# Kernel optimization log

Hardware: AMD Instinct MI355X
Metric: run time of the kernel (lower is better)

The kernel has to match this reference:

```python
import jax, jax.numpy as jnp
import numpy as np

B, T, D_IN, D_OUT, D_Z, D_H = 1024, 512, 64, 32, 32, 128
MIN_LV, MAX_LV = -10.0, 2.0
LOG2PI = float(np.log(2.0 * np.pi))
BETA_KL = 1.0


def _clamp(lv):
    return jnp.clip(lv, MIN_LV, MAX_LV)


def _mlp3(h, W1, b1, W2, b2, W3, b3):
    # depth=2 MLP: Linear->Tanh->Linear->Tanh->Linear
    h = jnp.tanh(h @ W1 + b1)
    h = jnp.tanh(h @ W2 + b2)
    return h @ W3 + b3


def setup_inputs() -> dict:
    key = jax.random.key(0)
    ks = iter(jax.random.split(key, 40))

    def lin(i, o):
        W = jax.random.normal(next(ks), (i, o), jnp.float32) / np.sqrt(i)
        b = 0.01 * jax.random.normal(next(ks), (o,), jnp.float32)
        return W, b

    inp = {}
    inp["x"] = jax.random.normal(next(ks), (B, T, D_IN), jnp.float32)
    inp["y_true"] = jax.random.normal(next(ks), (B, T, D_OUT), jnp.float32)
    for name, i, o in [("prior", D_Z + D_IN, 2 * D_Z),
                       ("post", D_Z + D_IN + D_OUT, 2 * D_Z),
                       ("emit", D_Z, 2 * D_OUT)]:
        W1, b1 = lin(i, D_H)
        W2, b2 = lin(D_H, D_H)
        W3, b3 = lin(D_H, o)
        inp[f"{name}_W1"], inp[f"{name}_b1"] = W1, b1
        inp[f"{name}_W2"], inp[f"{name}_b2"] = W2, b2
        inp[f"{name}_W3"], inp[f"{name}_b3"] = W3, b3
    inp["z0_mu"] = jnp.zeros((D_Z,), jnp.float32)
    inp["z0_logvar"] = jnp.zeros((D_Z,), jnp.float32)
    return inp


def reference(x, y_true,
              prior_W1, prior_b1, prior_W2, prior_b2, prior_W3, prior_b3,
              post_W1, post_b1, post_W2, post_b2, post_W3, post_b3,
              emit_W1, emit_b1, emit_W2, emit_b2, emit_W3, emit_b3,
              z0_mu, z0_logvar):
    Bc, Tc = x.shape[0], x.shape[1]
    # deterministic reparameterization noise (torch uses randn_like)
    ek = jax.random.key(42)
    eps0 = jax.random.normal(jax.random.fold_in(ek, 0), (Bc, D_Z), jnp.float32)
    eps = jax.random.normal(jax.random.fold_in(ek, 1), (Tc, Bc, D_Z), jnp.float32)

    z0 = z0_mu + jnp.exp(0.5 * _clamp(z0_logvar)) * eps0  # (B, Z)
    xs = jnp.swapaxes(x, 0, 1)       # (T, B, D_in)
    ys = jnp.swapaxes(y_true, 0, 1)  # (T, B, D_out)

    def step(z_prev, inp_t):
        x_t, y_t, e_t = inp_t
        p = _mlp3(jnp.concatenate([z_prev, x_t], -1),
                  prior_W1, prior_b1, prior_W2, prior_b2, prior_W3, prior_b3)
        mu_p, lv_p = jnp.split(p, 2, -1)
        lv_p = _clamp(lv_p)
        q = _mlp3(jnp.concatenate([z_prev, x_t, y_t], -1),
                  post_W1, post_b1, post_W2, post_b2, post_W3, post_b3)
        mu_q, lv_q = jnp.split(q, 2, -1)
        lv_q = _clamp(lv_q)
        z_t = mu_q + jnp.exp(0.5 * lv_q) * e_t
        em = _mlp3(z_t, emit_W1, emit_b1, emit_W2, emit_b2, emit_W3, emit_b3)
        mu_y, lv_y = jnp.split(em, 2, -1)
        lv_y = _clamp(lv_y)
        return z_t, (mu_y, lv_y, mu_q, lv_q, mu_p, lv_p)

    _, (mu_y, lv_y, mu_q, lv_q, mu_p, lv_p) = jax.lax.scan(step, z0, (xs, ys, eps))
    mu_y = jnp.swapaxes(mu_y, 0, 1)  # (B, T, D_out) == y_hat (sample=False)
    lv_y = jnp.swapaxes(lv_y, 0, 1)

    # Gaussian NLL (mean over B*T, sum over out_dim)
    nll = 0.5 * jnp.mean(jnp.sum(lv_y + (y_true - mu_y) ** 2 / jnp.exp(lv_y) + LOG2PI, -1))
    # KL(q || p) diag Gaussians (mean over T*B, sum over latent)
    var_q, var_p = jnp.exp(lv_q), jnp.exp(lv_p)
    kl = 0.5 * jnp.mean(jnp.sum(lv_p - lv_q + (var_q + (mu_q - mu_p) ** 2) / (var_p + 1e-12) - 1.0, -1))
    total = nll + BETA_KL * kl
    return mu_y, total, nll, kl
```

## Files before the change

kernel.cpp:

```cpp
#include <hip/hip_runtime.h>
#include <stdint.h>

#define Bdim 1024
#define Tdim 512
#define DIN  64
#define DOUT 32
#define DZ   32
#define DH   128
#define Msamp 4
#define NWG  256
#define NTHR 512
#define SP   144

using s16x8 = __attribute__((ext_vector_type(8))) short;
using f32x4 = __attribute__((ext_vector_type(4))) float;

#define MFMA(a, b, c) __builtin_amdgcn_mfma_f32_16x16x32_bf16((a), (b), (c), 0, 0, 0)

#define BAR() do { asm volatile("s_waitcnt lgkmcnt(0)" ::: "memory"); \
                   __builtin_amdgcn_s_barrier();                      \
                   asm volatile("" ::: "memory"); } while (0)

__host__ __device__ inline void tf2x32(unsigned k0, unsigned k1, unsigned c0, unsigned c1,
                                       unsigned &o0, unsigned &o1) {
  unsigned ks2 = k0 ^ k1 ^ 0x1BD11BDAu;
  unsigned x0 = c0 + k0, x1 = c1 + k1;
#define TFR(r) { x0 += x1; x1 = (x1 << (r)) | (x1 >> (32 - (r))); x1 ^= x0; }
  TFR(13) TFR(15) TFR(26) TFR(6)
  x0 += k1;  x1 += ks2 + 1u;
  TFR(17) TFR(29) TFR(16) TFR(24)
  x0 += ks2; x1 += k0 + 2u;
  TFR(13) TFR(15) TFR(26) TFR(6)
  x0 += k0;  x1 += k1 + 3u;
  TFR(17) TFR(29) TFR(16) TFR(24)
  x0 += k1;  x1 += ks2 + 4u;
  TFR(13) TFR(15) TFR(26) TFR(6)
  x0 += ks2; x1 += k0 + 5u;
#undef TFR
  o0 = x0; o1 = x1;
}

__device__ inline float erfinv_xla(float x) {
  float w = -log1pf(-x * x);
  float p;
  if (w < 5.0f) {
    w -= 2.5f;
    p = 2.81022636e-08f;
    p = fmaf(p, w, 3.43273939e-07f);
    p = fmaf(p, w, -3.5233877e-06f);
    p = fmaf(p, w, -4.39150654e-06f);
    p = fmaf(p, w, 0.00021858087f);
    p = fmaf(p, w, -0.00125372503f);
    p = fmaf(p, w, -0.00417768164f);
    p = fmaf(p, w, 0.246640727f);
    p = fmaf(p, w, 1.50140941f);
  } else {
    w = sqrtf(w) - 3.0f;
    p = -0.000200214257f;
    p = fmaf(p, w, 0.000100950558f);
    p = fmaf(p, w, 0.00134934322f);
    p = fmaf(p, w, -0.00367342844f);
    p = fmaf(p, w, 0.00573950773f);
    p = fmaf(p, w, -0.0076224613f);
    p = fmaf(p, w, 0.00943887047f);
    p = fmaf(p, w, 1.00167406f);
    p = fmaf(p, w, 2.83297682f);
  }
  return p * x;
}

__device__ inline float bits_to_normal(unsigned bits) {
  float f = __uint_as_float((bits >> 9) | 0x3f800000u) - 1.0f;
  float u = f * 2.0f - 0.99999994f;
  u = fmaxf(u, -0.99999994f);
  return 1.41421356f * erfinv_xla(u);
}

__device__ inline float jax_normal(unsigned k0, unsigned k1, unsigned idx) {
  unsigned o0, o1;
  tf2x32(k0, k1, 0u, idx, o0, o1);
  return bits_to_normal(o0 ^ o1);
}

__device__ inline float clampf(float v) { return fminf(fmaxf(v, -10.0f), 2.0f); }
__device__ inline float tanh_fast(float v) {
  float e = __expf(2.0f * v);
  return 1.0f - __fdividef(2.0f, e + 1.0f);
}
__device__ inline short f2bf(float x) {
  unsigned u = __float_as_uint(x);
  u = (u + 0x7fffu + ((u >> 16) & 1u)) >> 16;
  return (short)u;
}
__device__ inline float sel4(f32x4 v, int g) {
  float r = v[0];
  r = (g == 1) ? v[1] : r;
  r = (g == 2) ? v[2] : r;
  r = (g == 3) ? v[3] : r;
  return r;
}

__device__ inline s16x8 load_frag(const float* __restrict__ W, int N, int kt, int nt, int lane) {
  int k0 = kt * 32 + ((lane >> 4) << 3);
  int n  = nt * 16 + (lane & 15);
  s16x8 f;
#pragma unroll
  for (int e = 0; e < 8; ++e) f[e] = f2bf(W[(size_t)(k0 + e) * N + n]);
  return f;
}

__global__ __launch_bounds__(NTHR, 2) void dssm_main(
    const float* __restrict__ gx, const float* __restrict__ gy,
    const float* __restrict__ pW1, const float* __restrict__ pb1,
    const float* __restrict__ pW2, const float* __restrict__ pb2,
    const float* __restrict__ pW3, const float* __restrict__ pb3,
    const float* __restrict__ qW1, const float* __restrict__ qb1,
    const float* __restrict__ qW2, const float* __restrict__ qb2,
    const float* __restrict__ qW3, const float* __restrict__ qb3,
    const float* __restrict__ eW1, const float* __restrict__ eb1,
    const float* __restrict__ eW2, const float* __restrict__ eb2,
    const float* __restrict__ eW3, const float* __restrict__ eb3,
    const float* __restrict__ z0mu, const float* __restrict__ z0lv,
    float* __restrict__ gout, float* __restrict__ gws,
    unsigned ka0, unsigned ka1, unsigned kb0, unsigned kb1)
{
  __shared__ __align__(16) short in_pq[4 * SP];
  __shared__ __align__(16) short hpa[4 * SP], hqa[4 * SP], hea[4 * SP];
  __shared__ __align__(16) short hpb[4 * SP], hqb[4 * SP], heb[4 * SP];
  __shared__ float out_q2[4][32][2], out_p2[4][32][2], emit_o2[4][32][2];
  __shared__ float y_f32[4][128];
  __shared__ float epsb[2][128];

  const int tid  = threadIdx.x;
  const int w    = tid >> 6;
  const int lane = tid & 63;
  const int col  = lane & 15;
  const int g    = lane >> 4;
  const int wg   = blockIdx.x;
  const int base = wg * Msamp;

  s16x8 f1p[3], f1q[4], f1e, f2[16], f3[8];
#pragma unroll
  for (int i = 0; i < 16; ++i) f2[i] = (s16x8)(short)0;
#pragma unroll
  for (int i = 0; i < 8; ++i) f3[i] = (s16x8)(short)0;

#pragma unroll
  for (int kt = 0; kt < 3; ++kt) f1p[kt] = load_frag(pW1, DH, kt, w, lane);
#pragma unroll
  for (int kt = 0; kt < 4; ++kt) f1q[kt] = load_frag(qW1, DH, kt, w, lane);
  f1e = load_frag(eW1, DH, 0, w, lane);

  if (w < 2) {
#pragma unroll
    for (int nt = 0; nt < 4; ++nt)
#pragma unroll
      for (int kt = 0; kt < 4; ++kt) f2[nt * 4 + kt] = load_frag(pW2, DH, kt, w * 4 + nt, lane);
  } else if (w < 4) {
#pragma unroll
    for (int nt = 0; nt < 4; ++nt)
#pragma unroll
      for (int kt = 0; kt < 4; ++kt) f2[nt * 4 + kt] = load_frag(qW2, DH, kt, (w - 2) * 4 + nt, lane);
  } else if (w < 6) {
#pragma unroll
    for (int nt = 0; nt < 4; ++nt)
#pragma unroll
      for (int kt = 0; kt < 4; ++kt) f2[nt * 4 + kt] = load_frag(eW2, DH, kt, (w - 4) * 4 + nt, lane);
  }

  if (w < 4) {
#pragma unroll
    for (int kt = 0; kt < 4; ++kt) f3[kt] = load_frag(eW3, 2 * DOUT, kt, w, lane);
  } else if (w < 6) {
#pragma unroll
    for (int kt = 0; kt < 4; ++kt) { f3[kt] = load_frag(qW3, 2 * DZ, kt, w - 4, lane);
                                     f3[4 + kt] = load_frag(qW3, 2 * DZ, kt, w - 2, lane); }
  } else {
#pragma unroll
    for (int kt = 0; kt < 4; ++kt) { f3[kt] = load_frag(pW3, 2 * DZ, kt, w - 6, lane);
                                     f3[4 + kt] = load_frag(pW3, 2 * DZ, kt, w - 4, lane); }
  }

  const float b1p = pb1[w * 16 + col], b1q = qb1[w * 16 + col], b1e = eb1[w * 16 + col];
  float b2[4];
#pragma unroll
  for (int nt = 0; nt < 4; ++nt) {
    int n = ((w & 1) * 4 + nt) * 16 + col;
    b2[nt] = (w < 2) ? pb2[n] : (w < 4) ? qb2[n] : (w < 6) ? eb2[n] : 0.0f;
  }
  float b3a = 0.0f, b3b = 0.0f;
  if (w < 4)      { b3a = eb3[w * 16 + col]; }
  else if (w < 6) { b3a = qb3[(w - 4) * 16 + col]; b3b = qb3[32 + (w - 4) * 16 + col]; }
  else            { b3a = pb3[(w - 6) * 16 + col]; b3b = pb3[32 + (w - 6) * 16 + col]; }

  const s16x8* A1 = (const s16x8*)(in_pq + (col & 3) * SP) + g;
  const short* p2s = (w < 2) ? hpa : (w < 4) ? hqa : hea;
  const s16x8* A2 = (const s16x8*)(p2s + (col & 3) * SP) + g;
  short* p2d = (w < 2) ? hpb : (w < 4) ? hqb : heb;
  const short* p3s = (w < 4) ? heb : (w < 6) ? hqb : hpb;
  const s16x8* A3 = (const s16x8*)(p3s + (col & 3) * SP) + g;

  if (w < 4) {
    in_pq[w * SP + 32 + lane] = f2bf(gx[((size_t)(base + w) * Tdim) * DIN + lane]);
  } else if (w < 6) {
    int s = (w - 4) * 2 + (lane >> 5), j = lane & 31;
    float yv = gy[((size_t)(base + s) * Tdim) * DOUT + j];
    in_pq[s * SP + 96 + j] = f2bf(yv);
    y_f32[0][s * 32 + j] = yv;
  } else {
    int s = (w - 6) * 2 + (lane >> 5), zd = lane & 31;
    float e0 = jax_normal(ka0, ka1, (unsigned)(base + s) * 32u + (unsigned)zd);
    float lv = clampf(z0lv[zd]);
    in_pq[s * SP + zd] = f2bf(z0mu[zd] + __expf(0.5f * lv) * e0);
  }
  if (w == 0) epsb[0][lane] = jax_normal(kb0, kb1, (unsigned)base * 32u + lane);
  if (w == 1) epsb[0][64 + lane] = jax_normal(kb0, kb1, (unsigned)base * 32u + 64u + lane);
  BAR();

  float kl_acc = 0.0f, nll_acc = 0.0f;
  float xnext = 0.0f, ynext = 0.0f;

#pragma unroll 1
  for (int t = 0; t <= Tdim; ++t) {
    if (w < 4 && t < Tdim - 1)
      xnext = gx[((size_t)(base + w) * Tdim + (t + 1)) * DIN + lane];
    if ((w == 4 || w == 5) && t < Tdim - 1)
      ynext = gy[((size_t)(base + (w - 4) * 2 + (lane >> 5)) * Tdim + (t + 1)) * DOUT + (lane & 31)];

    {
      s16x8 a0 = A1[0], a1 = A1[4], a2 = A1[8], a3 = A1[12];
      f32x4 cE = {0.f, 0.f, 0.f, 0.f};
      cE = MFMA(a0, f1e, cE);
      hea[g * SP + w * 16 + col] = f2bf(tanh_fast(sel4(cE, g) + b1e));
      if (t < Tdim) {
        f32x4 cP = {0.f, 0.f, 0.f, 0.f}, cQ = {0.f, 0.f, 0.f, 0.f};
        cP = MFMA(a0, f1p[0], cP); cP = MFMA(a1, f1p[1], cP); cP = MFMA(a2, f1p[2], cP);
        cQ = MFMA(a0, f1q[0], cQ); cQ = MFMA(a1, f1q[1], cQ);
        cQ = MFMA(a2, f1q[2], cQ); cQ = MFMA(a3, f1q[3], cQ);
        hpa[g * SP + w * 16 + col] = f2bf(tanh_fast(sel4(cP, g) + b1p));
        hqa[g * SP + w * 16 + col] = f2bf(tanh_fast(sel4(cQ, g) + b1q));
      }
    }
    BAR();

    if (w < 6) {
      if (w >= 4 || t < Tdim) {
        s16x8 a0 = A2[0], a1 = A2[4], a2 = A2[8], a3 = A2[12];
        f32x4 d0 = {0.f,0.f,0.f,0.f}, d1 = {0.f,0.f,0.f,0.f},
              d2 = {0.f,0.f,0.f,0.f}, d3 = {0.f,0.f,0.f,0.f};
        d0 = MFMA(a0, f2[0],  d0); d0 = MFMA(a1, f2[1],  d0);
        d0 = MFMA(a2, f2[2],  d0); d0 = MFMA(a3, f2[3],  d0);
        d1 = MFMA(a0, f2[4],  d1); d1 = MFMA(a1, f2[5],  d1);
        d1 = MFMA(a2, f2[6],  d1); d1 = MFMA(a3, f2[7],  d1);
        d2 = MFMA(a0, f2[8],  d2); d2 = MFMA(a1, f2[9],  d2);
        d2 = MFMA(a2, f2[10], d2); d2 = MFMA(a3, f2[11], d2);
        d3 = MFMA(a0, f2[12], d3); d3 = MFMA(a1, f2[13], d3);
        d3 = MFMA(a2, f2[14], d3); d3 = MFMA(a3, f2[15], d3);
        int nb = (w & 1) * 4;
        p2d[g * SP + (nb + 0) * 16 + col] = f2bf(tanh_fast(sel4(d0, g) + b2[0]));
        p2d[g * SP + (nb + 1) * 16 + col] = f2bf(tanh_fast(sel4(d1, g) + b2[1]));
        p2d[g * SP + (nb + 2) * 16 + col] = f2bf(tanh_fast(sel4(d2, g) + b2[2]));
        p2d[g * SP + (nb + 3) * 16 + col] = f2bf(tanh_fast(sel4(d3, g) + b2[3]));
      }
    } else if (w == 6) {
      if (t >= 1) {
        float2 q0 = *(const float2*)&out_q2[g][col][0];
        float2 p0 = *(const float2*)&out_p2[g][col][0];
        float2 q1 = *(const float2*)&out_q2[g][col + 16][0];
        float2 p1 = *(const float2*)&out_p2[g][col + 16][0];
        float dm0 = q0.x - p0.x, dm1 = q1.x - p1.x;
        kl_acc += p0.y - q0.y + (__expf(q0.y) + dm0 * dm0) / (__expf(p0.y) + 1e-12f);
        kl_acc += p1.y - q1.y + (__expf(q1.y) + dm1 * dm1) / (__expf(p1.y) + 1e-12f);
      }
    } else {
      if (t >= 2) {
        float2 e0 = *(const float2*)&emit_o2[g][col][0];
        float2 e1 = *(const float2*)&emit_o2[g][col + 16][0];
        float y0 = y_f32[(t - 2) & 3][g * 32 + col];
        float y1 = y_f32[(t - 2) & 3][g * 32 + col + 16];
        float d0 = y0 - e0.x, d1 = y1 - e1.x;
        nll_acc += e0.y + d0 * d0 * __expf(-e0.y);
        nll_acc += e1.y + d1 * d1 * __expf(-e1.y);
      }
    }
    BAR();

    if (w < 4) {
      s16x8 a0 = A3[0], a1 = A3[4], a2 = A3[8], a3 = A3[12];
      f32x4 e = {0.f, 0.f, 0.f, 0.f};
      e = MFMA(a0, f3[0], e); e = MFMA(a1, f3[1], e);
      e = MFMA(a2, f3[2], e); e = MFMA(a3, f3[3], e);
      float v = sel4(e, g) + b3a;
      if (w < 2) {
        if (t >= 1)
          gout[((size_t)(base + g) * Tdim + (t - 1)) * DOUT + w * 16 + col] = v;
        emit_o2[g][w * 16 + col][0] = v;
      } else {
        emit_o2[g][(w - 2) * 16 + col][1] = clampf(v);
        if (t < Tdim - 1)
          epsb[(t + 1) & 1][(w - 2) * 64 + lane] =
              jax_normal(kb0, kb1, (unsigned)(t + 1) * 32768u + (unsigned)base * 32u + (w - 2) * 64u + lane);
      }
      if (t < Tdim - 1) in_pq[w * SP + 32 + lane] = f2bf(xnext);
    } else if (t < Tdim) {
      s16x8 a0 = A3[0], a1 = A3[4], a2 = A3[8], a3 = A3[12];
      f32x4 cM = {0.f,0.f,0.f,0.f}, cL = {0.f,0.f,0.f,0.f};
      cM = MFMA(a0, f3[0], cM); cM = MFMA(a1, f3[1], cM);
      cM = MFMA(a2, f3[2], cM); cM = MFMA(a3, f3[3], cM);
      cL = MFMA(a0, f3[4], cL); cL = MFMA(a1, f3[5], cL);
      cL = MFMA(a2, f3[6], cL); cL = MFMA(a3, f3[7], cL);
      float mu = sel4(cM, g) + b3a;
      float lv = clampf(sel4(cL, g) + b3b);
      int jc = (w & 1) * 16 + col;
      if (w < 6) {
        float z = mu + __expf(0.5f * lv) * epsb[t & 1][g * 32 + jc];
        in_pq[g * SP + jc] = f2bf(z);
        *(float2*)&out_q2[g][jc][0] = make_float2(mu, lv);
        if (t < Tdim - 1) {
          int s = (w - 4) * 2 + (lane >> 5), j = lane & 31;
          in_pq[s * SP + 96 + j] = f2bf(ynext);
          y_f32[(t + 1) & 3][s * 32 + j] = ynext;
        }
      } else {
        *(float2*)&out_p2[g][jc][0] = make_float2(mu, lv);
      }
    }
    BAR();
  }

  if (w == 7) {
    float2 e0 = *(const float2*)&emit_o2[g][col][0];
    float2 e1 = *(const float2*)&emit_o2[g][col + 16][0];
    float y0 = y_f32[(Tdim - 1) & 3][g * 32 + col];
    float y1 = y_f32[(Tdim - 1) & 3][g * 32 + col + 16];
    float d0 = y0 - e0.x, d1 = y1 - e1.x;
    nll_acc += e0.y + d0 * d0 * __expf(-e0.y);
    nll_acc += e1.y + d1 * d1 * __expf(-e1.y);
  }

  float vn = nll_acc, vk = kl_acc;
#pragma unroll
  for (int o = 32; o > 0; o >>= 1) { vn += __shfl_down(vn, o, 64); vk += __shfl_down(vk, o, 64); }
  if (w == 7 && lane == 0) gws[wg] = vn;
  if (w == 6 && lane == 0) gws[NWG + wg] = vk;
}

__global__ void dssm_fin(const float* __restrict__ gws, float* __restrict__ gout) {
  __shared__ float sb[8];
  int tid = threadIdx.x;
  int w = tid >> 6, lane = tid & 63;
  float vn = gws[tid], vk = gws[NWG + tid];
#pragma unroll
  for (int o = 32; o > 0; o >>= 1) { vn += __shfl_down(vn, o, 64); vk += __shfl_down(vk, o, 64); }
  if (lane == 0) { sb[w] = vn; sb[4 + w] = vk; }
  __syncthreads();
  if (tid == 0) {
    float sn = 0.f, sk = 0.f;
#pragma unroll
    for (int i = 0; i < 4; ++i) { sn += sb[i]; sk += sb[4 + i]; }
    const float inv = 1.0f / (float)((size_t)Bdim * Tdim);
    float nll = 0.5f * (sn * inv + (float)DOUT * 1.8378770664093453f);
    float kl  = 0.5f * (sk * inv - (float)DZ);
    size_t o0 = (size_t)Bdim * Tdim * DOUT;
    gout[o0 + 0] = nll + kl;
    gout[o0 + 1] = nll;
    gout[o0 + 2] = kl;
  }
}

extern "C" void kernel_launch(void* const* d_in, const int* in_sizes, int n_in,
                              void* d_out, int out_size, void* d_ws, size_t ws_size,
                              hipStream_t stream) {
  (void)in_sizes; (void)n_in; (void)out_size; (void)ws_size;
  const float* gx  = (const float*)d_in[0];
  const float* gy  = (const float*)d_in[1];
  const float* pW1 = (const float*)d_in[2];  const float* pb1 = (const float*)d_in[3];
  const float* pW2 = (const float*)d_in[4];  const float* pb2 = (const float*)d_in[5];
  const float* pW3 = (const float*)d_in[6];  const float* pb3 = (const float*)d_in[7];
  const float* qW1 = (const float*)d_in[8];  const float* qb1 = (const float*)d_in[9];
  const float* qW2 = (const float*)d_in[10]; const float* qb2 = (const float*)d_in[11];
  const float* qW3 = (const float*)d_in[12]; const float* qb3 = (const float*)d_in[13];
  const float* eW1 = (const float*)d_in[14]; const float* eb1 = (const float*)d_in[15];
  const float* eW2 = (const float*)d_in[16]; const float* eb2 = (const float*)d_in[17];
  const float* eW3 = (const float*)d_in[18]; const float* eb3 = (const float*)d_in[19];
  const float* z0mu = (const float*)d_in[20];
  const float* z0lv = (const float*)d_in[21];
  float* gout = (float*)d_out;
  float* gws  = (float*)d_ws;

  unsigned ka0, ka1, kb0, kb1;
  tf2x32(0u, 42u, 0u, 0u, ka0, ka1);
  tf2x32(0u, 42u, 0u, 1u, kb0, kb1);

  dssm_main<<<NWG, NTHR, 0, stream>>>(gx, gy,
      pW1, pb1, pW2, pb2, pW3, pb3,
      qW1, qb1, qW2, qb2, qW3, qb3,
      eW1, eb1, eW2, eb2, eW3, eb3,
      z0mu, z0lv, gout, gws, ka0, ka1, kb0, kb1);
  dssm_fin<<<1, 256, 0, stream>>>(gws, gout);
}
```

Baseline: 887.7 us.

## Double workgroup to 16 waves and rebalance MLP work per wave

Raises the block size from 8 to 16 waves and reassigns the work: waves 0-7 own the posterior layers 1-2, and waves 8-15 own the prior and emission layers 1-2. The layer-3 weights for posterior and prior are staged in shared-memory pools rather than held in registers. The change also batches the eps generation so four timesteps are produced every fourth step, and it spreads the KL/NLL accumulation across two waves with a shared-memory combine. The aim is to shorten the serial per-step critical path, since each wave now runs fewer MFMA chains between barriers. The cost is more barrier participants, higher register pressure with a launch bound of 4, and extra LDS reads for the layer-3 weights.

```diff
diff --git a/kernel.cpp b/kernel.cpp
--- a/kernel.cpp
+++ b/kernel.cpp
@@ -9,7 +9,7 @@
 #define DH   128
 #define Msamp 4
 #define NWG  256
-#define NTHR 512
+#define NTHR 1024
 #define SP   144
 
 using s16x8 = __attribute__((ext_vector_type(8))) short;
@@ -109,7 +109,7 @@
   return f;
 }
 
-__global__ __launch_bounds__(NTHR, 2) void dssm_main(
+__global__ __launch_bounds__(NTHR, 4) void dssm_main(
     const float* __restrict__ gx, const float* __restrict__ gy,
     const float* __restrict__ pW1, const float* __restrict__ pb1,
     const float* __restrict__ pW2, const float* __restrict__ pb2,
@@ -127,9 +127,12 @@
   __shared__ __align__(16) short in_pq[4 * SP];
   __shared__ __align__(16) short hpa[4 * SP], hqa[4 * SP], hea[4 * SP];
   __shared__ __align__(16) short hpb[4 * SP], hqb[4 * SP], heb[4 * SP];
+  __shared__ __align__(16) s16x8 poolQ3[16][64];
+  __shared__ __align__(16) s16x8 poolP3[16][64];
   __shared__ float out_q2[4][32][2], out_p2[4][32][2], emit_o2[4][32][2];
   __shared__ float y_f32[4][128];
-  __shared__ float epsb[2][128];
+  __shared__ float epsb[4][128];
+  __shared__ float redsb[4];
 
   const int tid  = threadIdx.x;
   const int w    = tid >> 6;
@@ -138,226 +141,237 @@
   const int g    = lane >> 4;
   const int wg   = blockIdx.x;
   const int base = wg * Msamp;
-
-  s16x8 f1p[3], f1q[4], f1e, f2[16], f3[8];
-#pragma unroll
-  for (int i = 0; i < 16; ++i) f2[i] = (s16x8)(short)0;
-#pragma unroll
-  for (int i = 0; i < 8; ++i) f3[i] = (s16x8)(short)0;
-
-#pragma unroll
-  for (int kt = 0; kt < 3; ++kt) f1p[kt] = load_frag(pW1, DH, kt, w, lane);
-#pragma unroll
-  for (int kt = 0; kt < 4; ++kt) f1q[kt] = load_frag(qW1, DH, kt, w, lane);
-  f1e = load_frag(eW1, DH, 0, w, lane);
-
-  if (w < 2) {
-#pragma unroll
-    for (int nt = 0; nt < 4; ++nt)
-#pragma unroll
-      for (int kt = 0; kt < 4; ++kt) f2[nt * 4 + kt] = load_frag(pW2, DH, kt, w * 4 + nt, lane);
-  } else if (w < 4) {
-#pragma unroll
-    for (int nt = 0; nt < 4; ++nt)
-#pragma unroll
-      for (int kt = 0; kt < 4; ++kt) f2[nt * 4 + kt] = load_frag(qW2, DH, kt, (w - 2) * 4 + nt, lane);
-  } else if (w < 6) {
-#pragma unroll
-    for (int nt = 0; nt < 4; ++nt)
-#pragma unroll
-      for (int kt = 0; kt < 4; ++kt) f2[nt * 4 + kt] = load_frag(eW2, DH, kt, (w - 4) * 4 + nt, lane);
-  }
-
-  if (w < 4) {
-#pragma unroll
-    for (int kt = 0; kt < 4; ++kt) f3[kt] = load_frag(eW3, 2 * DOUT, kt, w, lane);
-  } else if (w < 6) {
-#pragma unroll
-    for (int kt = 0; kt < 4; ++kt) { f3[kt] = load_frag(qW3, 2 * DZ, kt, w - 4, lane);
-                                     f3[4 + kt] = load_frag(qW3, 2 * DZ, kt, w - 2, lane); }
+  const int ww   = w & 7;
+  const int nt16 = ww * 16;
+
+  s16x8 fL1[4], fL2[4], fX[4];
+  if (w < 8) {
+#pragma unroll
+    for (int kt = 0; kt < 4; ++kt) fL1[kt] = load_frag(qW1, DH, kt, w, lane);
+#pragma unroll
+    for (int kt = 0; kt < 4; ++kt) fL2[kt] = load_frag(qW2, DH, kt, w, lane);
+    if (w >= 4) {
+#pragma unroll
+      for (int kt = 0; kt < 4; ++kt) fX[kt] = load_frag(eW3, 64, kt, w - 4, lane);
+    }
   } else {
 #pragma unroll
-    for (int kt = 0; kt < 4; ++kt) { f3[kt] = load_frag(pW3, 2 * DZ, kt, w - 6, lane);
-                                     f3[4 + kt] = load_frag(pW3, 2 * DZ, kt, w - 4, lane); }
-  }
-
-  const float b1p = pb1[w * 16 + col], b1q = qb1[w * 16 + col], b1e = eb1[w * 16 + col];
-  float b2[4];
-#pragma unroll
-  for (int nt = 0; nt < 4; ++nt) {
-    int n = ((w & 1) * 4 + nt) * 16 + col;
-    b2[nt] = (w < 2) ? pb2[n] : (w < 4) ? qb2[n] : (w < 6) ? eb2[n] : 0.0f;
-  }
-  float b3a = 0.0f, b3b = 0.0f;
-  if (w < 4)      { b3a = eb3[w * 16 + col]; }
-  else if (w < 6) { b3a = qb3[(w - 4) * 16 + col]; b3b = qb3[32 + (w - 4) * 16 + col]; }
-  else            { b3a = pb3[(w - 6) * 16 + col]; b3b = pb3[32 + (w - 6) * 16 + col]; }
-
-  const s16x8* A1 = (const s16x8*)(in_pq + (col & 3) * SP) + g;
-  const short* p2s = (w < 2) ? hpa : (w < 4) ? hqa : hea;
-  const s16x8* A2 = (const s16x8*)(p2s + (col & 3) * SP) + g;
-  short* p2d = (w < 2) ? hpb : (w < 4) ? hqb : heb;
-  const short* p3s = (w < 4) ? heb : (w < 6) ? hqb : hpb;
-  const s16x8* A3 = (const s16x8*)(p3s + (col & 3) * SP) + g;
+    for (int kt = 0; kt < 3; ++kt) fL1[kt] = load_frag(pW1, DH, kt, ww, lane);
+    fL1[3] = load_frag(eW1, DH, 0, ww, lane);
+#pragma unroll
+    for (int kt = 0; kt < 4; ++kt) fL2[kt] = load_frag(pW2, DH, kt, ww, lane);
+#pragma unroll
+    for (int kt = 0; kt < 4; ++kt) fX[kt]  = load_frag(eW2, DH, kt, ww, lane);
+  }
+  {
+    int s0 = 2 * ww;
+    if (w < 8) {
+      poolQ3[s0][lane]     = load_frag(qW3, 64, s0 & 3, s0 >> 2, lane);
+      poolQ3[s0 + 1][lane] = load_frag(qW3, 64, (s0 + 1) & 3, (s0 + 1) >> 2, lane);
+    } else {
+      poolP3[s0][lane]     = load_frag(pW3, 64, s0 & 3, s0 >> 2, lane);
+      poolP3[s0 + 1][lane] = load_frag(pW3, 64, (s0 + 1) & 3, (s0 + 1) >> 2, lane);
+    }
+  }
+
+  float b1, b2, b1e = 0.f, b2e = 0.f, b3m = 0.f, b3l = 0.f;
+  if (w < 8) {
+    b1 = qb1[nt16 + col]; b2 = qb2[nt16 + col];
+    if (w < 2)      { b3m = qb3[w * 16 + col];       b3l = qb3[32 + w * 16 + col]; }
+    else if (w < 4) { b3m = pb3[(w - 2) * 16 + col]; b3l = pb3[32 + (w - 2) * 16 + col]; }
+    else            { b3m = eb3[(w - 4) * 16 + col]; }
+  } else {
+    b1 = pb1[nt16 + col]; b2 = pb2[nt16 + col];
+    b1e = eb1[nt16 + col]; b2e = eb2[nt16 + col];
+  }
+
+  const int aoff = (col & 3) * SP + g * 8;
+  const short* A1  = in_pq + aoff;
+  const short* A2  = ((w < 8) ? hqa : hpa) + aoff;
+  const short* A2e = hea + aoff;
+  const short* A3  = ((w < 2) ? hqb : (w < 4) ? hpb : heb) + aoff;
 
   if (w < 4) {
     in_pq[w * SP + 32 + lane] = f2bf(gx[((size_t)(base + w) * Tdim) * DIN + lane]);
-  } else if (w < 6) {
-    int s = (w - 4) * 2 + (lane >> 5), j = lane & 31;
-    float yv = gy[((size_t)(base + s) * Tdim) * DOUT + j];
-    in_pq[s * SP + 96 + j] = f2bf(yv);
-    y_f32[0][s * 32 + j] = yv;
-  } else {
-    int s = (w - 6) * 2 + (lane >> 5), zd = lane & 31;
-    float e0 = jax_normal(ka0, ka1, (unsigned)(base + s) * 32u + (unsigned)zd);
-    float lv = clampf(z0lv[zd]);
-    in_pq[s * SP + zd] = f2bf(z0mu[zd] + __expf(0.5f * lv) * e0);
-  }
-  if (w == 0) epsb[0][lane] = jax_normal(kb0, kb1, (unsigned)base * 32u + lane);
-  if (w == 1) epsb[0][64 + lane] = jax_normal(kb0, kb1, (unsigned)base * 32u + 64u + lane);
+  } else if (w == 4 || w == 5) {
+    int off = (w - 4) * 64 + lane;
+    float yv = gy[((size_t)(base + (off >> 5)) * Tdim) * DOUT + (off & 31)];
+    in_pq[(off >> 5) * SP + 96 + (off & 31)] = f2bf(yv);
+    y_f32[0][off] = yv;
+  } else if (w == 6 || w == 7) {
+    int off = (w - 6) * 64 + lane;
+    float e0 = jax_normal(ka0, ka1, (unsigned)base * 32u + (unsigned)off);
+    float lv = clampf(z0lv[off & 31]);
+    in_pq[(off >> 5) * SP + (off & 31)] = f2bf(z0mu[off & 31] + __expf(0.5f * lv) * e0);
+  }
   BAR();
 
   float kl_acc = 0.0f, nll_acc = 0.0f;
-  float xnext = 0.0f, ynext = 0.0f;
+  float xn = 0.0f, yn = 0.0f;
 
 #pragma unroll 1
   for (int t = 0; t <= Tdim; ++t) {
     if (w < 4 && t < Tdim - 1)
-      xnext = gx[((size_t)(base + w) * Tdim + (t + 1)) * DIN + lane];
-    if ((w == 4 || w == 5) && t < Tdim - 1)
-      ynext = gy[((size_t)(base + (w - 4) * 2 + (lane >> 5)) * Tdim + (t + 1)) * DOUT + (lane & 31)];
-
+      xn = gx[((size_t)(base + w) * Tdim + (t + 1)) * DIN + lane];
+    if ((w == 4 || w == 5) && t < Tdim - 1) {
+      int off = (w - 4) * 64 + lane;
+      yn = gy[((size_t)(base + (off >> 5)) * Tdim + (t + 1)) * DOUT + (off & 31)];
+    }
+    if (w >= 8 && (t & 3) == 0 && t < Tdim) {
+      int k = (w - 8) >> 1, off = ((w - 8) & 1) * 64 + lane;
+      epsb[k][off] = jax_normal(kb0, kb1,
+          (unsigned)(t + k) * 32768u + (unsigned)base * 32u + (unsigned)off);
+    }
     {
-      s16x8 a0 = A1[0], a1 = A1[4], a2 = A1[8], a3 = A1[12];
-      f32x4 cE = {0.f, 0.f, 0.f, 0.f};
-      cE = MFMA(a0, f1e, cE);
-      hea[g * SP + w * 16 + col] = f2bf(tanh_fast(sel4(cE, g) + b1e));
-      if (t < Tdim) {
-        f32x4 cP = {0.f, 0.f, 0.f, 0.f}, cQ = {0.f, 0.f, 0.f, 0.f};
-        cP = MFMA(a0, f1p[0], cP); cP = MFMA(a1, f1p[1], cP); cP = MFMA(a2, f1p[2], cP);
-        cQ = MFMA(a0, f1q[0], cQ); cQ = MFMA(a1, f1q[1], cQ);
-        cQ = MFMA(a2, f1q[2], cQ); cQ = MFMA(a3, f1q[3], cQ);
-        hpa[g * SP + w * 16 + col] = f2bf(tanh_fast(sel4(cP, g) + b1p));
-        hqa[g * SP + w * 16 + col] = f2bf(tanh_fast(sel4(cQ, g) + b1q));
+      s16x8 a0 = *(const s16x8*)A1,        a1 = *(const s16x8*)(A1 + 32);
+      s16x8 a2 = *(const s16x8*)(A1 + 64), a3 = *(const s16x8*)(A1 + 96);
+      const f32x4 z4 = {0.f, 0.f, 0.f, 0.f};
+      if (w < 8) {
+        if (t < Tdim) {
+          f32x4 c = z4;
+          c = MFMA(a0, fL1[0], c); c = MFMA(a1, fL1[1], c);
+          c = MFMA(a2, fL1[2], c); c = MFMA(a3, fL1[3], c);
+          hqa[g * SP + nt16 + col] = f2bf(tanh_fast(sel4(c, g) + b1));
+        }
+      } else {
+        f32x4 cE = MFMA(a0, fL1[3], z4);
+        hea[g * SP + nt16 + col] = f2bf(tanh_fast(sel4(cE, g) + b1e));
+        if (t < Tdim) {
+          f32x4 c = z4;
+          c = MFMA(a0, fL1[0], c); c = MFMA(a1, fL1[1], c); c = MFMA(a2, fL1[2], c);
+          hpa[g * SP + nt16 + col] = f2bf(tanh_fast(sel4(c, g) + b1));
+        }
       }
     }
     BAR();
 
-    if (w < 6) {
-      if (w >= 4 || t < Tdim) {
-        s16x8 a0 = A2[0], a1 = A2[4], a2 = A2[8], a3 = A2[12];
-        f32x4 d0 = {0.f,0.f,0.f,0.f}, d1 = {0.f,0.f,0.f,0.f},
-              d2 = {0.f,0.f,0.f,0.f}, d3 = {0.f,0.f,0.f,0.f};
-        d0 = MFMA(a0, f2[0],  d0); d0 = MFMA(a1, f2[1],  d0);
-        d0 = MFMA(a2, f2[2],  d0); d0 = MFMA(a3, f2[3],  d0);
-        d1 = MFMA(a0, f2[4],  d1); d1 = MFMA(a1, f2[5],  d1);
-        d1 = MFMA(a2, f2[6],  d1); d1 = MFMA(a3, f2[7],  d1);
-        d2 = MFMA(a0, f2[8],  d2); d2 = MFMA(a1, f2[9],  d2);
-        d2 = MFMA(a2, f2[10], d2); d2 = MFMA(a3, f2[11], d2);
-        d3 = MFMA(a0, f2[12], d3); d3 = MFMA(a1, f2[13], d3);
-        d3 = MFMA(a2, f2[14], d3); d3 = MFMA(a3, f2[15], d3);
-        int nb = (w & 1) * 4;
-        p2d[g * SP + (nb + 0) * 16 + col] = f2bf(tanh_fast(sel4(d0, g) + b2[0]));
-        p2d[g * SP + (nb + 1) * 16 + col] = f2bf(tanh_fast(sel4(d1, g) + b2[1]));
-        p2d[g * SP + (nb + 2) * 16 + col] = f2bf(tanh_fast(sel4(d2, g) + b2[2]));
-        p2d[g * SP + (nb + 3) * 16 + col] = f2bf(tanh_fast(sel4(d3, g) + b2[3]));
+    {
+      const f32x4 z4 = {0.f, 0.f, 0.f, 0.f};
+      if (w < 8) {
+        if (t < Tdim) {
+          s16x8 a0 = *(const s16x8*)A2,        a1 = *(const s16x8*)(A2 + 32);
+          s16x8 a2 = *(const s16x8*)(A2 + 64), a3 = *(const s16x8*)(A2 + 96);
+          f32x4 c = z4;
+          c = MFMA(a0, fL2[0], c); c = MFMA(a1, fL2[1], c);
+          c = MFMA(a2, fL2[2], c); c = MFMA(a3, fL2[3], c);
+          hqb[g * SP + nt16 + col] = f2bf(tanh_fast(sel4(c, g) + b2));
+        }
+      } else {
+        s16x8 e0 = *(const s16x8*)A2e,        e1 = *(const s16x8*)(A2e + 32);
+        s16x8 e2 = *(const s16x8*)(A2e + 64), e3 = *(const s16x8*)(A2e + 96);
+        f32x4 ce = z4;
+        ce = MFMA(e0, fX[0], ce); ce = MFMA(e1, fX[1], ce);
+        ce = MFMA(e2, fX[2], ce); ce = MFMA(e3, fX[3], ce);
+        heb[g * SP + nt16 + col] = f2bf(tanh_fast(sel4(ce, g) + b2e));
+        if (t < Tdim) {
+          s16x8 a0 = *(const s16x8*)A2,        a1 = *(const s16x8*)(A2 + 32);
+          s16x8 a2 = *(const s16x8*)(A2 + 64), a3 = *(const s16x8*)(A2 + 96);
+          f32x4 c = z4;
+          c = MFMA(a0, fL2[0], c); c = MFMA(a1, fL2[1], c);
+          c = MFMA(a2, fL2[2], c); c = MFMA(a3, fL2[3], c);
+          hpb[g * SP + nt16 + col] = f2bf(tanh_fast(sel4(c, g) + b2));
+        }
       }
-    } else if (w == 6) {
-      if (t >= 1) {
-        float2 q0 = *(const float2*)&out_q2[g][col][0];
-        float2 p0 = *(const float2*)&out_p2[g][col][0];
-        float2 q1 = *(const float2*)&out_q2[g][col + 16][0];
-        float2 p1 = *(const float2*)&out_p2[g][col + 16][0];
-        float dm0 = q0.x - p0.x, dm1 = q1.x - p1.x;
-        kl_acc += p0.y - q0.y + (__expf(q0.y) + dm0 * dm0) / (__expf(p0.y) + 1e-12f);
-        kl_acc += p1.y - q1.y + (__expf(q1.y) + dm1 * dm1) / (__expf(p1.y) + 1e-12f);
+      if (w < 4 && t < Tdim - 1) in_pq[w * SP + 32 + lane] = f2bf(xn);
+      if ((w == 4 || w == 5) && t < Tdim - 1) {
+        int off = (w - 4) * 64 + lane;
+        in_pq[(off >> 5) * SP + 96 + (off & 31)] = f2bf(yn);
+        y_f32[(t + 1) & 3][off] = yn;
       }
-    } else {
-      if (t >= 2) {
-        float2 e0 = *(const float2*)&emit_o2[g][col][0];
-        float2 e1 = *(const float2*)&emit_o2[g][col + 16][0];
-        float y0 = y_f32[(t - 2) & 3][g * 32 + col];
-        float y1 = y_f32[(t - 2) & 3][g * 32 + col + 16];
-        float d0 = y0 - e0.x, d1 = y1 - e1.x;
-        nll_acc += e0.y + d0 * d0 * __expf(-e0.y);
-        nll_acc += e1.y + d1 * d1 * __expf(-e1.y);
+      if (w == 6 || w == 7) {
+        int off = (w - 6) * 64 + lane, s = off >> 5, zd = off & 31;
+        if (t >= 1) {
+          float2 q = *(const float2*)&out_q2[s][zd][0];
+          float2 p = *(const float2*)&out_p2[s][zd][0];
+          float dm = q.x - p.x;
+          kl_acc += p.y - q.y + (__expf(q.y) + dm * dm) / (__expf(p.y) + 1e-12f);
+        }
+        if (t >= 2) {
+          float2 e = *(const float2*)&emit_o2[s][zd][0];
+          float d = y_f32[(t - 2) & 3][off] - e.x;
+          nll_acc += e.y + d * d * __expf(-e.y);
+        }
       }
     }
     BAR();
 
-    if (w < 4) {
-      s16x8 a0 = A3[0], a1 = A3[4], a2 = A3[8], a3 = A3[12];
-      f32x4 e = {0.f, 0.f, 0.f, 0.f};
-      e = MFMA(a0, f3[0], e); e = MFMA(a1, f3[1], e);
-      e = MFMA(a2, f3[2], e); e = MFMA(a3, f3[3], e);
-      float v = sel4(e, g) + b3a;
-      if (w < 2) {
-        if (t >= 1)
-          gout[((size_t)(base + g) * Tdim + (t - 1)) * DOUT + w * 16 + col] = v;
-        emit_o2[g][w * 16 + col][0] = v;
-      } else {
-        emit_o2[g][(w - 2) * 16 + col][1] = clampf(v);
-        if (t < Tdim - 1)
-          epsb[(t + 1) & 1][(w - 2) * 64 + lane] =
-              jax_normal(kb0, kb1, (unsigned)(t + 1) * 32768u + (unsigned)base * 32u + (w - 2) * 64u + lane);
+    {
+      const f32x4 z4 = {0.f, 0.f, 0.f, 0.f};
+      if (w < 4) {
+        if (t < Tdim) {
+          s16x8 a0 = *(const s16x8*)A3,        a1 = *(const s16x8*)(A3 + 32);
+          s16x8 a2 = *(const s16x8*)(A3 + 64), a3 = *(const s16x8*)(A3 + 96);
+          const s16x8* pool = (w < 2) ? &poolQ3[0][0] : &poolP3[0][0];
+          const int mslot = (w & 1) * 4;
+          f32x4 cM = z4, cL = z4;
+          cM = MFMA(a0, pool[(mslot + 0) * 64 + lane], cM);
+          cM = MFMA(a1, pool[(mslot + 1) * 64 + lane], cM);
+          cM = MFMA(a2, pool[(mslot + 2) * 64 + lane], cM);
+          cM = MFMA(a3, pool[(mslot + 3) * 64 + lane], cM);
+          cL = MFMA(a0, pool[(8 + mslot + 0) * 64 + lane], cL);
+          cL = MFMA(a1, pool[(8 + mslot + 1) * 64 + lane], cL);
+          cL = MFMA(a2, pool[(8 + mslot + 2) * 64 + lane], cL);
+          cL = MFMA(a3, pool[(8 + mslot + 3) * 64 + lane], cL);
+          float mu = sel4(cM, g) + b3m;
+          float lv = clampf(sel4(cL, g) + b3l);
+          if (w < 2) {
+            float z = mu + __expf(0.5f * lv) * epsb[t & 3][g * 32 + w * 16 + col];
+            in_pq[g * SP + w * 16 + col] = f2bf(z);
+            *(float2*)&out_q2[g][w * 16 + col][0] = make_float2(mu, lv);
+          } else {
+            *(float2*)&out_p2[g][(w - 2) * 16 + col][0] = make_float2(mu, lv);
+          }
+        }
+      } else if (w < 8) {
+        s16x8 a0 = *(const s16x8*)A3,        a1 = *(const s16x8*)(A3 + 32);
+        s16x8 a2 = *(const s16x8*)(A3 + 64), a3 = *(const s16x8*)(A3 + 96);
+        f32x4 c = z4;
+        c = MFMA(a0, fX[0], c); c = MFMA(a1, fX[1], c);
+        c = MFMA(a2, fX[2], c); c = MFMA(a3, fX[3], c);
+        float v = sel4(c, g) + b3m;
+        if (w < 6) {
+          if (t >= 1)
+            gout[((size_t)(base + g) * Tdim + (t - 1)) * DOUT + (w - 4) * 16 + col] = v;
+          emit_o2[g][(w - 4) * 16 + col][0] = v;
+        } else {
+          emit_o2[g][(w - 6) * 16 + col][1] = clampf(v);
+        }
       }
-      if (t < Tdim - 1) in_pq[w * SP + 32 + lane] = f2bf(xnext);
-    } else if (t < Tdim) {
-      s16x8 a0 = A3[0], a1 = A3[4], a2 = A3[8], a3 = A3[12];
-      f32x4 cM = {0.f,0.f,0.f,0.f}, cL = {0.f,0.f,0.f,0.f};
-      cM = MFMA(a0, f3[0], cM); cM = MFMA(a1, f3[1], cM);
-      cM = MFMA(a2, f3[2], cM); cM = MFMA(a3, f3[3], cM);
-      cL = MFMA(a0, f3[4], cL); cL = MFMA(a1, f3[5], cL);
-      cL = MFMA(a2, f3[6], cL); cL = MFMA(a3, f3[7], cL);
-      float mu = sel4(cM, g) + b3a;
-      float lv = clampf(sel4(cL, g) + b3b);
-      int jc = (w & 1) * 16 + col;
-      if (w < 6) {
-        float z = mu + __expf(0.5f * lv) * epsb[t & 1][g * 32 + jc];
-        in_pq[g * SP + jc] = f2bf(z);
-        *(float2*)&out_q2[g][jc][0] = make_float2(mu, lv);
-        if (t < Tdim - 1) {
-          int s = (w - 4) * 2 + (lane >> 5), j = lane & 31;
-          in_pq[s * SP + 96 + j] = f2bf(ynext);
-          y_f32[(t + 1) & 3][s * 32 + j] = ynext;
-        }
-      } else {
-        *(float2*)&out_p2[g][jc][0] = make_float2(mu, lv);
-      }
     }
     BAR();
   }
 
-  if (w == 7) {
-    float2 e0 = *(const float2*)&emit_o2[g][col][0];
-    float2 e1 = *(const float2*)&emit_o2[g][col + 16][0];
-    float y0 = y_f32[(Tdim - 1) & 3][g * 32 + col];
-    float y1 = y_f32[(Tdim - 1) & 3][g * 32 + col + 16];
-    float d0 = y0 - e0.x, d1 = y1 - e1.x;
-    nll_acc += e0.y + d0 * d0 * __expf(-e0.y);
-    nll_acc += e1.y + d1 * d1 * __expf(-e1.y);
+  if (w == 6 || w == 7) {
+    int off = (w - 6) * 64 + lane, s = off >> 5, zd = off & 31;
+    float2 e = *(const float2*)&emit_o2[s][zd][0];
+    float d = y_f32[(Tdim - 1) & 3][off] - e.x;
+    nll_acc += e.y + d * d * __expf(-e.y);
   }
 
   float vn = nll_acc, vk = kl_acc;
 #pragma unroll
   for (int o = 32; o > 0; o >>= 1) { vn += __shfl_down(vn, o, 64); vk += __shfl_down(vk, o, 64); }
-  if (w == 7 && lane == 0) gws[wg] = vn;
-  if (w == 6 && lane == 0) gws[NWG + wg] = vk;
+  if ((w == 6 || w == 7) && lane == 0) { redsb[(w - 6) * 2] = vn; redsb[(w - 6) * 2 + 1] = vk; }
+  BAR();
+  if (tid == 0) {
+    gws[wg]       = redsb[0] + redsb[2];
+    gws[NWG + wg] = redsb[1] + redsb[3];
+  }
 }
 
 __global__ void dssm_fin(const float* __restrict__ gws, float* __restrict__ gout) {
-  __shared__ float sb[8];
+  __shared__ float sb2[8];
   int tid = threadIdx.x;
   int w = tid >> 6, lane = tid & 63;
   float vn = gws[tid], vk = gws[NWG + tid];
 #pragma unroll
   for (int o = 32; o > 0; o >>= 1) { vn += __shfl_down(vn, o, 64); vk += __shfl_down(vk, o, 64); }
-  if (lane == 0) { sb[w] = vn; sb[4 + w] = vk; }
+  if (lane == 0) { sb2[w] = vn; sb2[4 + w] = vk; }
   __syncthreads();
   if (tid == 0) {
     float sn = 0.f, sk = 0.f;
 #pragma unroll
-    for (int i = 0; i < 4; ++i) { sn += sb[i]; sk += sb[4 + i]; }
+    for (int i = 0; i < 4; ++i) { sn += sb2[i]; sk += sb2[4 + i]; }
     const float inv = 1.0f / (float)((size_t)Bdim * Tdim);
     float nll = 0.5f * (sn * inv + (float)DOUT * 1.8378770664093453f);
     float kl  = 0.5f * (sk * inv - (float)DZ);
```

Result: faster. 826.6 us (-6.9%).
